# Performance work log

Measured on AMD Instinct MI355X. Metric: run time of the kernel, lower is better.

## Reference

```python
import jax, jax.numpy as jnp
import numpy as np

L, P, D, NH, RBF, NL = 256, 1024, 256, 4, 50, 2
HD = D // NH
EPS = 1e-5


def _layernorm(x, g, b):
    mu = x.mean(-1, keepdims=True)
    var = ((x - mu) ** 2).mean(-1, keepdims=True)
    return (x - mu) * jax.lax.rsqrt(var + EPS) * g + b


def setup_inputs() -> dict:
    key = jax.random.key(0)
    ks = iter(jax.random.split(key, 64))
    def nrm(shape, s=0.02):
        return jax.random.normal(next(ks), shape, dtype=jnp.float32) * s
    inp = {
        "protein_features": jax.random.normal(next(ks), (1, P, 20), jnp.float32),
        "ligand_features": jax.random.normal(next(ks), (1, L, 20), jnp.float32),
        "protein_positions": jax.random.normal(next(ks), (1, P, 3), jnp.float32),
        "ligand_positions": jax.random.normal(next(ks), (1, L, 3), jnp.float32),
        "pair_rbf": jax.random.uniform(next(ks), (1, L, P, RBF), jnp.float32),
        # encoders
        "pe_w1": nrm((20, D)), "pe_b1": jnp.zeros((D,)),
        "pe_w2": nrm((D, D)), "pe_b2": jnp.zeros((D,)),
        "le_w1": nrm((20, D)), "le_b1": jnp.zeros((D,)),
        "le_w2": nrm((D, D)), "le_b2": jnp.zeros((D,)),
        # cross-attn layers stacked over NL
        "qw": nrm((NL, D, D)), "qb": jnp.zeros((NL, D)),
        "kw": nrm((NL, D, D)), "kb": jnp.zeros((NL, D)),
        "vw": nrm((NL, D, D)), "vb": jnp.zeros((NL, D)),
        "rw": nrm((NL, RBF, NH)), "rb": jnp.zeros((NL, NH)),
        "ow": nrm((NL, D, D)), "ob": jnp.zeros((NL, D)),
        "ln_g": jnp.ones((NL, D)), "ln_b": jnp.zeros((NL, D)),
        # gated pooling
        "pg_w1": nrm((D, D // 2)), "pg_b1": jnp.zeros((D // 2,)),
        "pg_w2": nrm((D // 2, 1)), "pg_b2": jnp.zeros((1,)),
        # heads
        "af_w1": nrm((D, D)), "af_b1": jnp.zeros((D,)),
        "af_w2": nrm((D, 1)), "af_b2": jnp.zeros((1,)),
        "cf_w1": nrm((D, D // 2)), "cf_b1": jnp.zeros((D // 2,)),
        "cf_w2": nrm((D // 2, 1)), "cf_b2": jnp.zeros((1,)),
        "iw1": nrm((2 * D + RBF, D)), "ib1": jnp.zeros((D,)),
        "iw2": nrm((D, 5)), "ib2": jnp.zeros((5,)),
    }
    return inp


def reference(protein_features, ligand_features, protein_positions, ligand_positions,
              pair_rbf, pe_w1, pe_b1, pe_w2, pe_b2, le_w1, le_b1, le_w2, le_b2,
              qw, qb, kw, kb, vw, vb, rw, rb, ow, ob, ln_g, ln_b,
              pg_w1, pg_b1, pg_w2, pg_b2, af_w1, af_b1, af_w2, af_b2,
              cf_w1, cf_b1, cf_w2, cf_b2, iw1, ib1, iw2, ib2):
    pf = protein_features[0]          # [P, 20]
    lf = ligand_features[0]           # [L, 20]
    rbf = pair_rbf[0]                 # [L, P, RBF]

    prot_h = jax.nn.silu(pf @ pe_w1 + pe_b1) @ pe_w2 + pe_b2   # [P, D]
    lig_h = jax.nn.silu(lf @ le_w1 + le_b1) @ le_w2 + le_b2    # [L, D]

    scale = float(HD) ** 0.5
    attn_w = None
    for i in range(NL):
        Q = (lig_h @ qw[i] + qb[i]).reshape(L, NH, HD)
        K = (prot_h @ kw[i] + kb[i]).reshape(P, NH, HD)
        V = (prot_h @ vw[i] + vb[i]).reshape(P, NH, HD)
        scores = jnp.einsum('lhd,phd->lph', Q, K) / scale      # [L, P, NH]
        scores = scores + (rbf @ rw[i] + rb[i])                # RBF additive bias per head
        attn_w = jax.nn.softmax(scores, axis=1)                # softmax over protein axis
        attended = jnp.einsum('lph,phd->lhd', attn_w, V).reshape(L, D)
        lig_h = _layernorm(lig_h + attended @ ow[i] + ob[i], ln_g[i], ln_b[i])

    gate_logits = jnp.tanh(lig_h @ pg_w1 + pg_b1) @ pg_w2 + pg_b2  # [L, 1]
    gate = jax.nn.softmax(gate_logits, axis=0)
    complex_repr = (gate * lig_h).sum(axis=0, keepdims=True)        # [1, D]

    pkd = jax.nn.silu(complex_repr @ af_w1 + af_b1) @ af_w2 + af_b2
    conf = jax.nn.sigmoid(jax.nn.silu(complex_repr @ cf_w1 + cf_b1) @ cf_w2 + cf_b2)
    docking_score = pkd * conf

    lig_exp = jnp.broadcast_to(lig_h[:, None, :], (L, P, D))
    prot_exp = jnp.broadcast_to(prot_h[None, :, :], (L, P, D))
    pair_input = jnp.concatenate([lig_exp, prot_exp, rbf], axis=-1)  # [L, P, 2D+RBF]
    imap = jax.nn.sigmoid(jax.nn.silu(pair_input @ iw1 + ib1) @ iw2 + ib2)

    attn_out = attn_w.mean(axis=-1).reshape(1, L * P)
    return (docking_score, pkd, conf, imap[None], attn_out)
```

## Files before the change

### kernel.cpp

```cpp
#include <hip/hip_runtime.h>
#include <math.h>

#define LN_ 256
#define PN_ 1024
#define DN_ 256
#define NH_ 4
#define RBF_N 50
#define NL_ 2
#define HD_ 64
#define EPSV 1e-5f
#define LP_ (LN_ * PN_)

__device__ __forceinline__ float fast_sigmoid(float x){ return 1.f/(1.f+__expf(-x)); }
__device__ __forceinline__ float fast_silu(float x){ return x/(1.f+__expf(-x)); }

struct GSeg {
  const float* A; const float* W; const float* bias; float* C;
  int K; int act; int transOut;
};
struct GArgs { GSeg s[3]; int b0, b1; };

__global__ __launch_bounds__(256) void gemm8(GArgs ga)
{
  extern __shared__ float sA[];
  int bid = blockIdx.x;
  int si = (bid < ga.b0) ? 0 : (bid < ga.b1 ? 1 : 2);
  int base = (si == 0) ? 0 : ((si == 1) ? ga.b0 : ga.b1);
  GSeg sg = ga.s[si];
  int row0 = (bid - base) * 8;
  int K = sg.K;
  int t = threadIdx.x;
  for (int idx = t; idx < 8 * K; idx += 256) {
    int r = idx / K, k = idx - r * K;
    sA[idx] = sg.A[(size_t)(row0 + r) * K + k];
  }
  __syncthreads();
  float acc[8];
  float bv = sg.bias ? sg.bias[t] : 0.f;
  #pragma unroll
  for (int r = 0; r < 8; r++) acc[r] = bv;
  for (int k = 0; k < K; k++) {
    float w = sg.W[(size_t)k * DN_ + t];
    #pragma unroll
    for (int r = 0; r < 8; r++) acc[r] = fmaf(sA[r * K + k], w, acc[r]);
  }
  #pragma unroll
  for (int r = 0; r < 8; r++) {
    float v = acc[r];
    if (sg.act == 1) v = fast_silu(v);
    if (sg.transOut) sg.C[(size_t)t * PN_ + row0 + r] = v;
    else             sg.C[(size_t)(row0 + r) * DN_ + t] = v;
  }
}

__global__ __launch_bounds__(256) void rbf_transpose(
    const float* __restrict__ rbf, float* __restrict__ rbfT)
{
  __shared__ float ld[256][RBF_N + 1];
  int t = threadIdx.x;
  size_t base = (size_t)blockIdx.x << 8;
  const float* src = rbf + base * RBF_N;
  for (int i = 0; i < RBF_N; i++) {
    int fl = i * 256 + t;
    int row = fl / RBF_N, col = fl - row * RBF_N;
    ld[row][col] = src[fl];
  }
  __syncthreads();
  for (int k = 0; k < RBF_N; k++)
    rbfT[(size_t)k * LP_ + base + t] = ld[t][k];
}

__global__ __launch_bounds__(256) void scores_softmax_l(
    const float* __restrict__ Q, const float* __restrict__ Kt,
    const float* __restrict__ rbfT, const float* __restrict__ rw,
    const float* __restrict__ rb, float* __restrict__ attn,
    float* __restrict__ amean)
{
  int l = blockIdx.x, t = threadIdx.x, lane = t & 63, wv = t >> 6;
  __shared__ float qs[DN_];
  __shared__ float rws[NH_][RBF_N];
  __shared__ float redm[16], reds[16];
  qs[t] = Q[(size_t)l * DN_ + t];
  if (t < RBF_N * NH_) rws[t & 3][t >> 2] = rw[t];
  __syncthreads();

  float sc[NH_][4];
  for (int i = 0; i < 4; i++) {
    int p = t + (i << 8);
    size_t idx = ((size_t)l << 10) + p;
    float s2[NH_] = {0.f, 0.f, 0.f, 0.f};
    #pragma unroll 10
    for (int k = 0; k < RBF_N; k++) {
      float rv = rbfT[(size_t)k * LP_ + idx];
      s2[0] = fmaf(rv, rws[0][k], s2[0]);
      s2[1] = fmaf(rv, rws[1][k], s2[1]);
      s2[2] = fmaf(rv, rws[2][k], s2[2]);
      s2[3] = fmaf(rv, rws[3][k], s2[3]);
    }
    #pragma unroll
    for (int h = 0; h < NH_; h++) {
      const float* kp = Kt + ((size_t)(h << 6) << 10) + p;
      float a = 0.f;
      #pragma unroll 8
      for (int d = 0; d < HD_; d++) a = fmaf(qs[(h << 6) + d], kp[(size_t)d << 10], a);
      sc[h][i] = a * 0.125f + s2[h] + rb[h];
    }
  }

  float mh[NH_];
  #pragma unroll
  for (int h = 0; h < NH_; h++) {
    float m = fmaxf(fmaxf(sc[h][0], sc[h][1]), fmaxf(sc[h][2], sc[h][3]));
    for (int o = 32; o > 0; o >>= 1) m = fmaxf(m, __shfl_xor(m, o));
    if (lane == 0) redm[h * 4 + wv] = m;
  }
  __syncthreads();
  #pragma unroll
  for (int h = 0; h < NH_; h++)
    mh[h] = fmaxf(fmaxf(redm[h * 4 + 0], redm[h * 4 + 1]),
                  fmaxf(redm[h * 4 + 2], redm[h * 4 + 3]));

  float e[NH_][4], inv[NH_];
  #pragma unroll
  for (int h = 0; h < NH_; h++) {
    float s = 0.f;
    #pragma unroll
    for (int i = 0; i < 4; i++) { e[h][i] = __expf(sc[h][i] - mh[h]); s += e[h][i]; }
    for (int o = 32; o > 0; o >>= 1) s += __shfl_xor(s, o);
    if (lane == 0) reds[h * 4 + wv] = s;
  }
  __syncthreads();
  #pragma unroll
  for (int h = 0; h < NH_; h++)
    inv[h] = 1.f / (reds[h * 4 + 0] + reds[h * 4 + 1] + reds[h * 4 + 2] + reds[h * 4 + 3]);

  #pragma unroll
  for (int h = 0; h < NH_; h++)
    for (int i = 0; i < 4; i++)
      attn[(((size_t)(l << 2) + h) << 10) + t + (i << 8)] = e[h][i] * inv[h];

  if (amean) {
    for (int i = 0; i < 4; i++) {
      float s = e[0][i] * inv[0] + e[1][i] * inv[1] + e[2][i] * inv[2] + e[3][i] * inv[3];
      amean[((size_t)l << 10) + t + (i << 8)] = s * 0.25f;
    }
  }
}

__global__ __launch_bounds__(256) void attend_proj_ln(
    const float* __restrict__ attn, const float* __restrict__ V,
    const float* __restrict__ ow, const float* __restrict__ ob,
    const float* __restrict__ g, const float* __restrict__ bb,
    float* __restrict__ lig)
{
  int l = blockIdx.x, t = threadIdx.x, lane = t & 63, wv = t >> 6;
  int h = t >> 6, d = t & 63;
  __shared__ float as[DN_];
  __shared__ float red[8];
  const float* aw = attn + (((size_t)(l << 2) + h) << 10);
  const float* Vp = V + (h << 6) + d;
  float acc = 0.f;
  #pragma unroll 8
  for (int p = 0; p < PN_; p++) acc = fmaf(aw[p], Vp[(size_t)p << 8], acc);
  as[t] = acc;
  __syncthreads();
  float acc2 = ob[t];
  #pragma unroll 4
  for (int k = 0; k < DN_; k++) acc2 = fmaf(as[k], ow[(size_t)(k << 8) + t], acc2);
  float x = lig[((size_t)l << 8) + t] + acc2;
  float sm = x;
  for (int o = 32; o > 0; o >>= 1) sm += __shfl_xor(sm, o);
  if (lane == 0) red[wv] = sm;
  __syncthreads();
  float mu = (red[0] + red[1] + red[2] + red[3]) * (1.f / DN_);
  float dx = x - mu;
  float v = dx * dx;
  for (int o = 32; o > 0; o >>= 1) v += __shfl_xor(v, o);
  if (lane == 0) red[4 + wv] = v;
  __syncthreads();
  float var = (red[4] + red[5] + red[6] + red[7]) * (1.f / DN_);
  lig[((size_t)l << 8) + t] = dx * (1.f / sqrtf(var + EPSV)) * g[t] + bb[t];
}

__global__ __launch_bounds__(128) void gate_logits_k(
    const float* __restrict__ lig, const float* __restrict__ w1,
    const float* __restrict__ b1, const float* __restrict__ w2,
    const float* __restrict__ b2, float* __restrict__ glog)
{
  int l = blockIdx.x, n = threadIdx.x, lane = n & 63, wv = n >> 6;
  __shared__ float ls[DN_];
  __shared__ float red[2];
  ls[n] = lig[(size_t)l * DN_ + n];
  ls[n + 128] = lig[(size_t)l * DN_ + n + 128];
  __syncthreads();
  float acc = b1[n];
  #pragma unroll 4
  for (int k = 0; k < DN_; k++) acc = fmaf(ls[k], w1[k * 128 + n], acc);
  float part = tanhf(acc) * w2[n];
  for (int o = 32; o > 0; o >>= 1) part += __shfl_xor(part, o);
  if (lane == 0) red[wv] = part;
  __syncthreads();
  if (n == 0) glog[l] = red[0] + red[1] + b2[0];
}

__global__ __launch_bounds__(256) void pool_heads(
    const float* __restrict__ lig, const float* __restrict__ glog,
    const float* __restrict__ afw1, const float* __restrict__ afb1,
    const float* __restrict__ afw2, const float* __restrict__ afb2,
    const float* __restrict__ cfw1, const float* __restrict__ cfb1,
    const float* __restrict__ cfw2, const float* __restrict__ cfb2,
    float* __restrict__ out)
{
  __shared__ float wsh[LN_];
  __shared__ float cr[DN_];
  __shared__ float h1s[DN_];
  __shared__ float h2s[128];
  __shared__ float red[8];
  int t = threadIdx.x, lane = t & 63, wv = t >> 6;
  float x = glog[t];
  float m = x;
  for (int o = 32; o > 0; o >>= 1) m = fmaxf(m, __shfl_xor(m, o));
  if (lane == 0) red[wv] = m;
  __syncthreads();
  m = fmaxf(fmaxf(red[0], red[1]), fmaxf(red[2], red[3]));
  float e = __expf(x - m);
  float s = e;
  for (int o = 32; o > 0; o >>= 1) s += __shfl_xor(s, o);
  if (lane == 0) red[4 + wv] = s;
  __syncthreads();
  s = red[4] + red[5] + red[6] + red[7];
  wsh[t] = e / s;
  __syncthreads();
  float acc = 0.f;
  #pragma unroll 4
  for (int l2 = 0; l2 < LN_; l2++) acc = fmaf(wsh[l2], lig[(size_t)l2 * DN_ + t], acc);
  cr[t] = acc;
  __syncthreads();
  float a = afb1[t];
  #pragma unroll 4
  for (int d = 0; d < DN_; d++) a = fmaf(cr[d], afw1[d * DN_ + t], a);
  h1s[t] = fast_silu(a);
  if (t < 128) {
    float c = cfb1[t];
    #pragma unroll 4
    for (int d = 0; d < DN_; d++) c = fmaf(cr[d], cfw1[d * 128 + t], c);
    h2s[t] = fast_silu(c);
  }
  __syncthreads();
  float pp = h1s[t] * afw2[t];
  for (int o = 32; o > 0; o >>= 1) pp += __shfl_xor(pp, o);
  if (lane == 0) red[wv] = pp;
  float cp = (t < 128) ? h2s[t] * cfw2[t] : 0.f;
  for (int o = 32; o > 0; o >>= 1) cp += __shfl_xor(cp, o);
  if (lane == 0) red[4 + wv] = cp;
  __syncthreads();
  if (t == 0) {
    float pkd = red[0] + red[1] + red[2] + red[3] + afb2[0];
    float cl  = red[4] + red[5] + red[6] + red[7] + cfb2[0];
    float conf = fast_sigmoid(cl);
    out[0] = pkd * conf;
    out[1] = pkd;
    out[2] = conf;
  }
}

__global__ __launch_bounds__(256, 4) void pair_main2(
    const float* __restrict__ A, const float* __restrict__ BT,
    const float* __restrict__ rbfT, const float* __restrict__ Wr,
    const float* __restrict__ w2, const float* __restrict__ ib2,
    float* __restrict__ imap)
{
  int t = threadIdx.x;
  int bid = blockIdx.x;
  int l = bid >> 2;
  int p = ((bid & 3) << 8) + t;
  size_t idx = ((size_t)l << 10) + p;
  const float* Ar = A + (l << 8);
  float acc[5];
  #pragma unroll
  for (int o = 0; o < 5; o++) acc[o] = ib2[o];

  for (int dt = 0; dt < 4; dt++) {
    int d0 = dt << 6;
    float h[64];
    #pragma unroll
    for (int j = 0; j < 64; j++)
      h[j] = Ar[d0 + j] + BT[(size_t)(d0 + j) * PN_ + p];

    #pragma unroll 2
    for (int k = 0; k < RBF_N; k++) {
      float rv = rbfT[(size_t)k * LP_ + idx];
      const float* wr = Wr + k * DN_ + d0;
      #pragma unroll
      for (int j = 0; j < 64; j++)
        h[j] = fmaf(rv, wr[j], h[j]);
    }

    #pragma unroll
    for (int j = 0; j < 64; j++) {
      float sh = fast_silu(h[j]);
      const float* w2r = w2 + (size_t)(d0 + j) * 5;
      #pragma unroll
      for (int o = 0; o < 5; o++) acc[o] = fmaf(sh, w2r[o], acc[o]);
    }
  }
  float* op = imap + idx * 5;
  #pragma unroll
  for (int o = 0; o < 5; o++) op[o] = fast_sigmoid(acc[o]);
}

extern "C" void kernel_launch(void* const* d_in, const int* in_sizes, int n_in,
                              void* d_out, int out_size, void* d_ws, size_t ws_size,
                              hipStream_t stream)
{
  const float* pf    = (const float*)d_in[0];
  const float* lf    = (const float*)d_in[1];
  const float* rbf   = (const float*)d_in[4];
  const float* pe_w1 = (const float*)d_in[5];
  const float* pe_b1 = (const float*)d_in[6];
  const float* pe_w2 = (const float*)d_in[7];
  const float* pe_b2 = (const float*)d_in[8];
  const float* le_w1 = (const float*)d_in[9];
  const float* le_b1 = (const float*)d_in[10];
  const float* le_w2 = (const float*)d_in[11];
  const float* le_b2 = (const float*)d_in[12];
  const float* qw = (const float*)d_in[13];
  const float* qb = (const float*)d_in[14];
  const float* kw = (const float*)d_in[15];
  const float* kb = (const float*)d_in[16];
  const float* vw = (const float*)d_in[17];
  const float* vb = (const float*)d_in[18];
  const float* rw = (const float*)d_in[19];
  const float* rb = (const float*)d_in[20];
  const float* ow = (const float*)d_in[21];
  const float* ob = (const float*)d_in[22];
  const float* ln_g = (const float*)d_in[23];
  const float* ln_b = (const float*)d_in[24];
  const float* pg_w1 = (const float*)d_in[25];
  const float* pg_b1 = (const float*)d_in[26];
  const float* pg_w2 = (const float*)d_in[27];
  const float* pg_b2 = (const float*)d_in[28];
  const float* af_w1 = (const float*)d_in[29];
  const float* af_b1 = (const float*)d_in[30];
  const float* af_w2 = (const float*)d_in[31];
  const float* af_b2 = (const float*)d_in[32];
  const float* cf_w1 = (const float*)d_in[33];
  const float* cf_b1 = (const float*)d_in[34];
  const float* cf_w2 = (const float*)d_in[35];
  const float* cf_b2 = (const float*)d_in[36];
  const float* iw1 = (const float*)d_in[37];
  const float* ib1 = (const float*)d_in[38];
  const float* iw2 = (const float*)d_in[39];
  const float* ib2 = (const float*)d_in[40];

  float* out = (float*)d_out;

  float* w = (float*)d_ws;
  size_t off = 0;
  float* prot_h = w + off; off += (size_t)PN_ * DN_;
  float* lig_h  = w + off; off += (size_t)LN_ * DN_;
  float* ph1    = w + off; off += (size_t)PN_ * DN_;
  float* lh1    = w + off; off += (size_t)LN_ * DN_;
  float* Qb     = w + off; off += (size_t)LN_ * DN_;
  float* Kt     = w + off; off += (size_t)DN_ * PN_;
  float* Vb     = w + off; off += (size_t)PN_ * DN_;
  float* attn   = w + off; off += (size_t)LN_ * NH_ * PN_;
  float* pairA  = w + off; off += (size_t)LN_ * DN_;
  float* glog   = w + off; off += LN_;
  off = (off + 255) & ~(size_t)255;
  float* rbfT   = w + off; off += (size_t)RBF_N * LP_;

  const int PB = PN_ / 8;
  const int LB = LN_ / 8;
  const size_t smax = 8 * DN_ * sizeof(float);

  rbf_transpose<<<LP_ / 256, 256, 0, stream>>>(rbf, rbfT);

  {
    GArgs ga;
    ga.s[0] = { pf, pe_w1, pe_b1, ph1, 20, 1, 0 };
    ga.s[1] = { lf, le_w1, le_b1, lh1, 20, 1, 0 };
    ga.s[2] = ga.s[1];
    ga.b0 = PB; ga.b1 = PB + LB;
    gemm8<<<PB + LB, 256, smax, stream>>>(ga);
  }
  {
    GArgs ga;
    ga.s[0] = { ph1, pe_w2, pe_b2, prot_h, DN_, 0, 0 };
    ga.s[1] = { lh1, le_w2, le_b2, lig_h, DN_, 0, 0 };
    ga.s[2] = ga.s[1];
    ga.b0 = PB; ga.b1 = PB + LB;
    gemm8<<<PB + LB, 256, smax, stream>>>(ga);
  }

  for (int i = 0; i < NL_; i++) {
    const size_t wo = (size_t)i * DN_ * DN_;
    {
      GArgs ga;
      ga.s[0] = { lig_h,  qw + wo, qb + i * DN_, Qb, DN_, 0, 0 };
      ga.s[1] = { prot_h, kw + wo, kb + i * DN_, Kt, DN_, 0, 1 };
      ga.s[2] = { prot_h, vw + wo, vb + i * DN_, Vb, DN_, 0, 0 };
      ga.b0 = LB; ga.b1 = LB + PB;
      gemm8<<<LB + 2 * PB, 256, smax, stream>>>(ga);
    }
    scores_softmax_l<<<LN_, 256, 0, stream>>>(
        Qb, Kt, rbfT, rw + (size_t)i * RBF_N * NH_, rb + i * NH_, attn,
        (i == NL_ - 1) ? (out + 3 + (size_t)LN_ * PN_ * 5) : nullptr);
    attend_proj_ln<<<LN_, 256, 0, stream>>>(attn, Vb, ow + wo, ob + i * DN_,
                                            ln_g + i * DN_, ln_b + i * DN_, lig_h);
  }

  gate_logits_k<<<LN_, 128, 0, stream>>>(lig_h, pg_w1, pg_b1, pg_w2, pg_b2, glog);
  pool_heads<<<1, 256, 0, stream>>>(lig_h, glog, af_w1, af_b1, af_w2, af_b2,
                                    cf_w1, cf_b1, cf_w2, cf_b2, out);

  {
    GArgs ga;
    ga.s[0] = { lig_h,  iw1,                       ib1,     pairA, DN_, 0, 0 };
    ga.s[1] = { prot_h, iw1 + (size_t)DN_ * DN_,   nullptr, Kt,    DN_, 0, 1 };
    ga.s[2] = ga.s[1];
    ga.b0 = LB; ga.b1 = LB + PB;
    gemm8<<<LB + PB, 256, smax, stream>>>(ga);
  }

  pair_main2<<<LP_ / 256, 256, 0, stream>>>(
      pairA, Kt, rbfT, iw1 + (size_t)2 * DN_ * DN_, iw2, ib2, out + 3);
}
```

Before: 732.7 us.

## Compute pair RBF projection with bf16 MFMA and double-buffered protein tiles

Replaces the scalar per-thread pair kernel with an MFMA-based kernel. The RBF-by-weight product is computed in bf16 with 16x16x32 MFMA instructions, reading the raw rbf tensor directly into shared memory rather than the transposed copy. The protein-side projection tiles are double-buffered through LDS, and the 5-output head is reduced with cross-lane shuffles. This removes the large FP32 FMA load of the pair stage at the cost of bf16 rounding of the rbf values and weights, and it adds a small weight-packing kernel. The rbf transpose kernel is still launched even though the new kernel no longer reads its output.

```diff
diff --git a/kernel.cpp b/kernel.cpp
--- a/kernel.cpp
+++ b/kernel.cpp
@@ -11,8 +11,16 @@
 #define EPSV 1e-5f
 #define LP_ (LN_ * PN_)
 
+typedef __attribute__((ext_vector_type(8))) short bf16x8;
+typedef __attribute__((ext_vector_type(4))) float f32x4;
+
 __device__ __forceinline__ float fast_sigmoid(float x){ return 1.f/(1.f+__expf(-x)); }
 __device__ __forceinline__ float fast_silu(float x){ return x/(1.f+__expf(-x)); }
+__device__ __forceinline__ short f2bf(float x){
+  union { float f; unsigned u; } v; v.f = x;
+  unsigned r = v.u + 0x7FFF + ((v.u >> 16) & 1);
+  return (short)(r >> 16);
+}
 
 struct GSeg {
   const float* A; const float* W; const float* bias; float* C;
@@ -62,12 +70,20 @@
   const float* src = rbf + base * RBF_N;
   for (int i = 0; i < RBF_N; i++) {
     int fl = i * 256 + t;
-    int row = fl / RBF_N, col = fl - row * RBF_N;
-    ld[row][col] = src[fl];
+    int row = fl / RBF_N, colk = fl - row * RBF_N;
+    ld[row][colk] = src[fl];
   }
   __syncthreads();
   for (int k = 0; k < RBF_N; k++)
     rbfT[(size_t)k * LP_ + base + t] = ld[t][k];
+}
+
+__global__ __launch_bounds__(256) void wr_pack(
+    const float* __restrict__ Wr, short* __restrict__ WT)
+{
+  int d = threadIdx.x;
+  for (int k = 0; k < 64; k++)
+    WT[d * 64 + k] = (k < RBF_N) ? f2bf(Wr[k * DN_ + d]) : (short)0;
 }
 
 __global__ __launch_bounds__(256) void scores_softmax_l(
@@ -264,49 +280,129 @@
   }
 }
 
-__global__ __launch_bounds__(256, 4) void pair_main2(
+#define RSTR 72
+#define BTP2 133
+union PairSMem {
+  short R[128 * RSTR];
+  float B[2][16 * BTP2];
+};
+__global__ __launch_bounds__(512, 6) void pair_main4(
     const float* __restrict__ A, const float* __restrict__ BT,
-    const float* __restrict__ rbfT, const float* __restrict__ Wr,
+    const float* __restrict__ rbf, const short* __restrict__ WT,
     const float* __restrict__ w2, const float* __restrict__ ib2,
     float* __restrict__ imap)
 {
+  __shared__ PairSMem u;
+  __shared__ float sw2[DN_ * 5];
+  __shared__ float sAl[DN_];
+
   int t = threadIdx.x;
+  int lane = t & 63, wid = t >> 6;
   int bid = blockIdx.x;
-  int l = bid >> 2;
-  int p = ((bid & 3) << 8) + t;
-  size_t idx = ((size_t)l << 10) + p;
-  const float* Ar = A + (l << 8);
-  float acc[5];
-  #pragma unroll
-  for (int o = 0; o < 5; o++) acc[o] = ib2[o];
-
-  for (int dt = 0; dt < 4; dt++) {
-    int d0 = dt << 6;
-    float h[64];
-    #pragma unroll
-    for (int j = 0; j < 64; j++)
-      h[j] = Ar[d0 + j] + BT[(size_t)(d0 + j) * PN_ + p];
-
-    #pragma unroll 2
-    for (int k = 0; k < RBF_N; k++) {
-      float rv = rbfT[(size_t)k * LP_ + idx];
-      const float* wr = Wr + k * DN_ + d0;
+  int l = bid >> 3;
+  int p0 = (bid & 7) << 7;
+
+  {
+    unsigned* rz = (unsigned*)u.R;
+    #pragma unroll
+    for (int i = 0; i < 9; i++) rz[t + i * 512] = 0u;
+  }
+  __syncthreads();
+  {
+    const float* src = rbf + ((size_t)(l << 10) + p0) * RBF_N;
+    #pragma unroll
+    for (int i = 0; i < 13; i++) {
+      int idx = t + i * 512;
+      if (idx < 128 * RBF_N) {
+        int row = idx / RBF_N, k = idx - row * RBF_N;
+        u.R[row * RSTR + k] = f2bf(src[idx]);
+      }
+    }
+  }
+  for (int i = t; i < DN_ * 5; i += 512) sw2[i] = w2[i];
+  if (t < DN_) sAl[t] = A[((size_t)l << 8) + t];
+  __syncthreads();
+
+  int m = lane & 15, gq = lane >> 4;
+  bf16x8 a0 = *(const bf16x8*)&u.R[(wid * 16 + m) * RSTR + 0 + gq * 8];
+  bf16x8 a1 = *(const bf16x8*)&u.R[(wid * 16 + m) * RSTR + 32 + gq * 8];
+  __syncthreads();
+
+  int srow = t >> 7, scol = t & 127;
+  #pragma unroll
+  for (int i = 0; i < 4; i++)
+    u.B[0][(srow + 4 * i) * BTP2 + scol] =
+        BT[(size_t)(srow + 4 * i) * PN_ + p0 + scol];
+  __syncthreads();
+
+  float acc5[4][5];
+  #pragma unroll
+  for (int r = 0; r < 4; r++)
+    #pragma unroll
+    for (int o = 0; o < 5; o++) acc5[r][o] = 0.f;
+
+  int cur = 0;
+  for (int nt = 0; nt < 16; nt++) {
+    float ld0 = 0.f, ld1 = 0.f, ld2 = 0.f, ld3 = 0.f;
+    if (nt < 15) {
+      const float* bsrc = BT + (size_t)((nt + 1) * 16 + srow) * PN_ + p0 + scol;
+      ld0 = bsrc[0];
+      ld1 = bsrc[(size_t)4 * PN_];
+      ld2 = bsrc[(size_t)8 * PN_];
+      ld3 = bsrc[(size_t)12 * PN_];
+    }
+
+    int n = nt * 16 + m;
+    bf16x8 b0 = *(const bf16x8*)&WT[n * 64 + gq * 8];
+    bf16x8 b1 = *(const bf16x8*)&WT[n * 64 + 32 + gq * 8];
+    f32x4 acc = {0.f, 0.f, 0.f, 0.f};
+    acc = __builtin_amdgcn_mfma_f32_16x16x32_bf16(a0, b0, acc, 0, 0, 0);
+    acc = __builtin_amdgcn_mfma_f32_16x16x32_bf16(a1, b1, acc, 0, 0, 0);
+    float bA = sAl[n];
+    const float* bp = &u.B[cur][m * BTP2 + wid * 16 + gq * 4];
+    #pragma unroll
+    for (int r = 0; r < 4; r++) {
+      float h = acc[r] + bA + bp[r];
+      float sh = fast_silu(h);
       #pragma unroll
-      for (int j = 0; j < 64; j++)
-        h[j] = fmaf(rv, wr[j], h[j]);
-    }
-
-    #pragma unroll
-    for (int j = 0; j < 64; j++) {
-      float sh = fast_silu(h[j]);
-      const float* w2r = w2 + (size_t)(d0 + j) * 5;
+      for (int o = 0; o < 5; o++)
+        acc5[r][o] = fmaf(sh, sw2[n * 5 + o], acc5[r][o]);
+    }
+    __syncthreads();
+    if (nt < 15) {
+      float* bd = &u.B[cur ^ 1][srow * BTP2 + scol];
+      bd[0 * 4 * BTP2] = ld0;
+      bd[1 * 4 * BTP2] = ld1;
+      bd[2 * 4 * BTP2] = ld2;
+      bd[3 * 4 * BTP2] = ld3;
+      __syncthreads();
+      cur ^= 1;
+    }
+  }
+
+  #pragma unroll
+  for (int r = 0; r < 4; r++)
+    #pragma unroll
+    for (int o = 0; o < 5; o++) {
+      float v = acc5[r][o];
+      v += __shfl_xor(v, 1);
+      v += __shfl_xor(v, 2);
+      v += __shfl_xor(v, 4);
+      v += __shfl_xor(v, 8);
+      acc5[r][o] = v;
+    }
+
+  if (m < 5) {
+    float bo = ib2[m];
+    #pragma unroll
+    for (int r = 0; r < 4; r++) {
+      float v = 0.f;
       #pragma unroll
-      for (int o = 0; o < 5; o++) acc[o] = fmaf(sh, w2r[o], acc[o]);
-    }
-  }
-  float* op = imap + idx * 5;
-  #pragma unroll
-  for (int o = 0; o < 5; o++) op[o] = fast_sigmoid(acc[o]);
+      for (int o = 0; o < 5; o++) if (m == o) v = acc5[r][o];
+      int p = p0 + wid * 16 + gq * 4 + r;
+      imap[((size_t)(l << 10) + p) * 5 + m] = fast_sigmoid(v + bo);
+    }
+  }
 }
 
 extern "C" void kernel_launch(void* const* d_in, const int* in_sizes, int n_in,
@@ -368,6 +464,8 @@
   float* pairA  = w + off; off += (size_t)LN_ * DN_;
   float* glog   = w + off; off += LN_;
   off = (off + 255) & ~(size_t)255;
+  float* WrBF   = w + off; off += (size_t)DN_ * 64 / 2;
+  off = (off + 255) & ~(size_t)255;
   float* rbfT   = w + off; off += (size_t)RBF_N * LP_;
 
   const int PB = PN_ / 8;
@@ -375,6 +473,7 @@
   const size_t smax = 8 * DN_ * sizeof(float);
 
   rbf_transpose<<<LP_ / 256, 256, 0, stream>>>(rbf, rbfT);
+  wr_pack<<<1, 256, 0, stream>>>(iw1 + (size_t)2 * DN_ * DN_, (short*)WrBF);
 
   {
     GArgs ga;
@@ -423,6 +522,6 @@
     gemm8<<<LB + PB, 256, smax, stream>>>(ga);
   }
 
-  pair_main2<<<LP_ / 256, 256, 0, stream>>>(
-      pairA, Kt, rbfT, iw1 + (size_t)2 * DN_ * DN_, iw2, ib2, out + 3);
-}
+  pair_main4<<<(LN_ * PN_) / 128, 512, 0, stream>>>(
+      pairA, Kt, rbf, (const short*)WrBF, iw2, ib2, out + 3);
+}
```

Measured after the change: 715.2 us. -2.4%, faster.
